# Kernel tuning notes

Measured on AMD Instinct MI355X. Metric: run time of the kernel, lower is better.

Reference implementation:

```python
import jax, jax.numpy as jnp
import numpy as np

BATCH = 65536
CHANNELS = 64
SPLIT1 = 32
SPLIT2 = 32
DEGREE = 10


def _de_casteljau(t, coeffs):
    """Evaluate Bernstein polynomials at t via De Casteljau.
    t: [N], coeffs: [N, d+1] -> [N]."""
    t = t[:, None]
    y = coeffs
    for _ in range(coeffs.shape[1] - 1):
        y = (1.0 - t) * y[:, :-1] + t * y[:, 1:]
    return y[:, 0]


def setup_inputs() -> dict:
    key = jax.random.key(0)
    k1, k2, k3 = jax.random.split(key, 3)
    x = jax.random.normal(k1, (BATCH, CHANNELS), dtype=jnp.float32)
    # subnet: Linear(SPLIT1 -> SPLIT2*(DEGREE+2)) ; W stored as [out, in] like torch
    out_dim = SPLIT2 * (DEGREE + 2)
    W = jax.random.normal(k2, (out_dim, SPLIT1), dtype=jnp.float32) * 0.05
    b = jax.random.normal(k3, (out_dim,), dtype=jnp.float32) * 0.05
    return {"x": x, "W": W, "b": b}


def reference(x, W, b):
    x1 = x[:, :SPLIT1]
    x2 = x[:, SPLIT1:]

    # subnet + reshape to per-spline params: [B*SPLIT2, DEGREE+2]
    s = (x1 @ W.T + b).reshape(-1, DEGREE + 2)
    coeff_raw = s[:, :DEGREE]
    widths = s[:, DEGREE]
    heights = s[:, DEGREE + 1]

    # monotone normalized Bernstein coefficients in [0, 1]
    cs = jnp.cumsum(jax.nn.softplus(coeff_raw), axis=-1)
    coeffs = jnp.concatenate([jnp.zeros_like(cs[:, :1]), cs], axis=-1)
    coeffs = coeffs / coeffs[:, -1:]

    widths = jax.nn.softplus(widths)
    widths = widths + 0.1 * jnp.sign(widths)
    heights = heights + 0.1 * jnp.sign(heights)

    xf = x2.reshape(-1)                    # [B*SPLIT2]
    t = xf / widths + 0.5
    tc = jnp.clip(t, 0.0, 1.0)             # l-region -> 0, r-region -> 1

    # derivative coefficients: degree * (c[1:] - c[:-1])
    deriv = DEGREE * _de_casteljau(tc, coeffs[:, 1:] - coeffs[:, :-1])
    ym = _de_casteljau(tc, coeffs)

    # branchless l / m / r regions (same math as the masked torch version)
    y = jnp.where(t < 0.0, t * deriv,
                  jnp.where(t > 1.0, 1.0 + (t - 1.0) * deriv, ym))
    y = (y - 0.5) * heights

    return jnp.concatenate([x1, y.reshape(-1, SPLIT2)], axis=1)
```

## Files before the change

kernel.cpp:

```cpp
#include <hip/hip_runtime.h>


typedef short v8s  __attribute__((ext_vector_type(8)));
typedef float f32x4 __attribute__((ext_vector_type(4)));
typedef float f32x2 __attribute__((ext_vector_type(2)));

#define LOG2E 1.44269504088896340736f
#define LN2   0.69314718055994530942f

__device__ __forceinline__ short f2bf(float f) {
    union { float f; unsigned u; } v; v.f = f;
    return (short)((v.u + 0x7FFFu + ((v.u >> 16) & 1u)) >> 16);
}

__device__ __forceinline__ float bf2f(short h) {
    union { unsigned u; float f; } v; v.u = ((unsigned)(unsigned short)h) << 16;
    return v.f;
}

__device__ __forceinline__ float sgn01(float x) {
    return (x > 0.f) ? 1.f : ((x < 0.f) ? -1.f : 0.f);
}

__device__ __forceinline__ float softplus_l2(float x) {
    return __log2f(1.0f + exp2f(x * LOG2E));
}

__device__ __forceinline__ float softplus_f(float x) {
    return __logf(1.0f + __expf(x));
}
__device__ __forceinline__ float spline_eval(const float* sv, float xf) {
    float cn[11];
    cn[0] = 0.f;
    float run = 0.f;
#pragma unroll
    for (int j = 0; j < 10; ++j) { run += softplus_f(sv[j]); cn[j + 1] = run; }
    const float inv = __fdividef(1.f, run);
    const float wd = softplus_f(sv[10]) + 0.1f;
    float hg = sv[11];
    hg += 0.1f * sgn01(hg);
    const float t   = __fdividef(xf, wd) + 0.5f;
    const float tc  = fminf(fmaxf(t, 0.f), 1.f);
#pragma unroll
    for (int n = 10; n >= 2; --n) {
#pragma unroll
        for (int i = 0; i < n; ++i) cn[i] += tc * (cn[i + 1] - cn[i]);
    }
    const float db    = cn[1] - cn[0];
    const float deriv = 10.f * db * inv;
    const float ym    = fmaf(tc, db, cn[0]) * inv;
    float y = (t < 0.f) ? (t * deriv)
            : ((t > 1.f) ? fmaf(t - 1.f, deriv, 1.f) : ym);
    return (y - 0.5f) * hg;
}

__global__ void prep_w(const float* __restrict__ W, short* __restrict__ wsH,
                       short* __restrict__ wsL) {
    const int g = blockIdx.x * 256 + threadIdx.x;
    if (g < 12288) {
        const int o = g >> 5;
        const int k = g & 31;
        const float w = W[g];
        const short hi = f2bf(w);
        const int off = (k >> 3) * 3072 + o * 8 + (k & 7);
        wsH[off] = hi;
        wsL[off] = f2bf(w - bf2f(hi));
    }
}

__global__ __launch_bounds__(256) void bern_spline_fast(
    const float* __restrict__ x, const short* __restrict__ wsH,
    const short* __restrict__ wsL, const float* __restrict__ bias,
    float* __restrict__ out)
{
    __shared__ float sl[4 * 16 * 100];

    const int tid  = threadIdx.x;
    const int wave = tid >> 6;
    const int lane = tid & 63;
    const int cbit = blockIdx.x & 1;
    const int block_row = (blockIdx.x >> 1) * 64;

    const int row16 = lane & 15;
    const int kq    = lane >> 4;
    const int arow  = block_row + wave * 16 + row16;

    const f32x4 a0 = *(const f32x4*)(x + (size_t)arow * 64 + kq * 8);
    const f32x4 a1 = *(const f32x4*)(x + (size_t)arow * 64 + kq * 8 + 4);
    v8s ah, al;
#pragma unroll
    for (int e = 0; e < 4; ++e) {
        const short h0 = f2bf(a0[e]);
        ah[e] = h0;     al[e] = f2bf(a0[e] - bf2f(h0));
        const short h1 = f2bf(a1[e]);
        ah[e + 4] = h1; al[e + 4] = f2bf(a1[e] - bf2f(h1));
    }

    float* swv = sl + wave * 1600;
    const f32x4 zero4 = {0.f, 0.f, 0.f, 0.f};

    v8s bh0[6], bl0[6];
#pragma unroll
    for (int ot = 0; ot < 6; ++ot) {
        const int boff = kq * 3072 + ((cbit * 12 + ot) * 16 + row16) * 8;
        bh0[ot] = *(const v8s*)(wsH + boff);
        bl0[ot] = *(const v8s*)(wsL + boff);
    }

#pragma unroll
    for (int ot = 0; ot < 6; ++ot) {
        f32x4 c = __builtin_amdgcn_mfma_f32_16x16x32_bf16(al, bh0[ot], zero4, 0, 0, 0);
        c = __builtin_amdgcn_mfma_f32_16x16x32_bf16(ah, bl0[ot], c, 0, 0, 0);
        c = __builtin_amdgcn_mfma_f32_16x16x32_bf16(ah, bh0[ot], c, 0, 0, 0);
#pragma unroll
        for (int r = 0; r < 4; ++r)
            swv[(kq * 4 + r) * 100 + ot * 16 + row16] = c[r];
    }

    v8s bh1[6], bl1[6];
#pragma unroll
    for (int ot = 0; ot < 6; ++ot) {
        const int boff = kq * 3072 + ((cbit * 12 + 6 + ot) * 16 + row16) * 8;
        bh1[ot] = *(const v8s*)(wsH + boff);
        bl1[ot] = *(const v8s*)(wsL + boff);
    }

#pragma unroll
    for (int hf = 0; hf < 2; ++hf) {
        if (hf == 1) {
#pragma unroll
            for (int ot = 0; ot < 6; ++ot) {
                f32x4 c = __builtin_amdgcn_mfma_f32_16x16x32_bf16(al, bh1[ot], zero4, 0, 0, 0);
                c = __builtin_amdgcn_mfma_f32_16x16x32_bf16(ah, bl1[ot], c, 0, 0, 0);
                c = __builtin_amdgcn_mfma_f32_16x16x32_bf16(ah, bh1[ot], c, 0, 0, 0);
#pragma unroll
                for (int r = 0; r < 4; ++r)
                    swv[(kq * 4 + r) * 100 + ot * 16 + row16] = c[r];
            }
        }

        const int cg0 = cbit * 16 + hf * 8 + 2 * kq;
        const f32x2 xf2 = *(const f32x2*)(x + (size_t)arow * 64 + 32 + cg0);

        const float* sp = swv + row16 * 100 + 2 * kq * 12;
        const f32x4 sA0 = *(const f32x4*)(sp);
        const f32x4 sA1 = *(const f32x4*)(sp + 4);
        const f32x4 sA2 = *(const f32x4*)(sp + 8);
        const f32x4 sB0 = *(const f32x4*)(sp + 12);
        const f32x4 sB1 = *(const f32x4*)(sp + 16);
        const f32x4 sB2 = *(const f32x4*)(sp + 20);
        const float* bp = bias + cg0 * 12;
        const f32x4 bA0 = *(const f32x4*)(bp);
        const f32x4 bA1 = *(const f32x4*)(bp + 4);
        const f32x4 bA2 = *(const f32x4*)(bp + 8);
        const f32x4 bB0 = *(const f32x4*)(bp + 12);
        const f32x4 bB1 = *(const f32x4*)(bp + 16);
        const f32x4 bB2 = *(const f32x4*)(bp + 20);

        float svA[12], svB[12];
#pragma unroll
        for (int e = 0; e < 4; ++e) {
            svA[e]     = sA0[e] + bA0[e];
            svA[e + 4] = sA1[e] + bA1[e];
            svA[e + 8] = sA2[e] + bA2[e];
            svB[e]     = sB0[e] + bB0[e];
            svB[e + 4] = sB1[e] + bB1[e];
            svB[e + 8] = sB2[e] + bB2[e];
        }

        float cnA[11], cnB[11];
        cnA[0] = 0.f; cnB[0] = 0.f;
        float runA = 0.f, runB = 0.f;
#pragma unroll
        for (int j = 0; j < 10; ++j) {
            runA += softplus_l2(svA[j]); cnA[j + 1] = runA;
            runB += softplus_l2(svB[j]); cnB[j + 1] = runB;
        }
        const float invA = __fdividef(1.f, runA);
        const float invB = __fdividef(1.f, runB);

        const float wdA = fmaf(LN2, softplus_l2(svA[10]), 0.1f);
        const float wdB = fmaf(LN2, softplus_l2(svB[10]), 0.1f);
        float hgA = svA[11]; hgA += 0.1f * sgn01(hgA);
        float hgB = svB[11]; hgB += 0.1f * sgn01(hgB);

        const float tA  = __fdividef(xf2[0], wdA) + 0.5f;
        const float tB  = __fdividef(xf2[1], wdB) + 0.5f;
        const float tcA = fminf(fmaxf(tA, 0.f), 1.f);
        const float tcB = fminf(fmaxf(tB, 0.f), 1.f);

#pragma unroll
        for (int n = 10; n >= 2; --n) {
#pragma unroll
            for (int i = 0; i < n; ++i) {
                cnA[i] += tcA * (cnA[i + 1] - cnA[i]);
                cnB[i] += tcB * (cnB[i + 1] - cnB[i]);
            }
        }
        const float dbA = cnA[1] - cnA[0];
        const float dbB = cnB[1] - cnB[0];
        const float derA = 10.f * dbA * invA;
        const float derB = 10.f * dbB * invB;
        const float ymA = fmaf(tcA, dbA, cnA[0]) * invA;
        const float ymB = fmaf(tcB, dbB, cnB[0]) * invB;

        float yA = (tA < 0.f) ? (tA * derA)
                 : ((tA > 1.f) ? fmaf(tA - 1.f, derA, 1.f) : ymA);
        float yB = (tB < 0.f) ? (tB * derB)
                 : ((tB > 1.f) ? fmaf(tB - 1.f, derB, 1.f) : ymB);

        f32x2 y2;
        y2[0] = (yA - 0.5f) * hgA;
        y2[1] = (yB - 0.5f) * hgB;
        *(f32x2*)(out + (size_t)arow * 64 + 32 + cg0) = y2;
    }

    if (cbit == 0) {
        for (int i = tid; i < 512; i += 256) {
            const int r = i >> 3, q = i & 7;
            *(f32x4*)(out + (size_t)(block_row + r) * 64 + q * 4) =
                *(const f32x4*)(x + (size_t)(block_row + r) * 64 + q * 4);
        }
    }
}

__global__ __launch_bounds__(256) void bern_spline_fallback(
    const float* __restrict__ x, const float* __restrict__ W,
    const float* __restrict__ bias, float* __restrict__ out)
{
    __shared__ short Wh[12288];
    __shared__ short Wl[12288];
    __shared__ float bl[384];
    __shared__ float sl[4 * 16 * 100];

    const int tid  = threadIdx.x;
    const int wave = tid >> 6;
    const int lane = tid & 63;
    const int block_row = blockIdx.x * 64;

    for (int g = tid; g < 12288; g += 256) {
        const int o = g >> 5;
        const int k = g & 31;
        const float w = W[g];
        const short hi = f2bf(w);
        Wh[(k >> 3) * 3072 + o * 8 + (k & 7)] = hi;
        Wl[(k >> 3) * 3072 + o * 8 + (k & 7)] = f2bf(w - bf2f(hi));
    }
    for (int g = tid; g < 384; g += 256) bl[g] = bias[g];
    __syncthreads();

    for (int i = tid; i < 512; i += 256) {
        const int r = i >> 3, q = i & 7;
        *(f32x4*)(out + (size_t)(block_row + r) * 64 + q * 4) =
            *(const f32x4*)(x + (size_t)(block_row + r) * 64 + q * 4);
    }

    const int row16 = lane & 15;
    const int kq    = lane >> 4;
    const int arow  = block_row + wave * 16 + row16;
    const f32x4 a0 = *(const f32x4*)(x + (size_t)arow * 64 + kq * 8);
    const f32x4 a1 = *(const f32x4*)(x + (size_t)arow * 64 + kq * 8 + 4);
    v8s ah, al;
#pragma unroll
    for (int e = 0; e < 4; ++e) {
        const short h0 = f2bf(a0[e]);
        ah[e] = h0;     al[e] = f2bf(a0[e] - bf2f(h0));
        const short h1 = f2bf(a1[e]);
        ah[e + 4] = h1; al[e + 4] = f2bf(a1[e] - bf2f(h1));
    }

    float* swv = sl + wave * 1600;
    const f32x4 zero4 = {0.f, 0.f, 0.f, 0.f};

    for (int qt = 0; qt < 4; ++qt) {
        f32x4 acc[6];
#pragma unroll
        for (int ot = 0; ot < 6; ++ot) {
            const int otg = qt * 6 + ot;
            const int boff = kq * 3072 + (otg * 16 + row16) * 8;
            const v8s bh  = *(const v8s*)(Wh + boff);
            const v8s blo = *(const v8s*)(Wl + boff);
            f32x4 c = __builtin_amdgcn_mfma_f32_16x16x32_bf16(al, bh, zero4, 0, 0, 0);
            c = __builtin_amdgcn_mfma_f32_16x16x32_bf16(ah, blo, c, 0, 0, 0);
            acc[ot] = __builtin_amdgcn_mfma_f32_16x16x32_bf16(ah, bh, c, 0, 0, 0);
        }
#pragma unroll
        for (int ot = 0; ot < 6; ++ot)
#pragma unroll
            for (int r = 0; r < 4; ++r)
                swv[(kq * 4 + r) * 100 + ot * 16 + row16] = acc[ot][r];

#pragma unroll
        for (int p = 0; p < 2; ++p) {
            const int idx = p * 64 + lane;
            const int cl  = idx & 7;
            const int rr  = idx >> 3;
            const int cg  = qt * 8 + cl;

            const float* sp = swv + rr * 100 + cl * 12;
            const f32x4 s0 = *(const f32x4*)(sp);
            const f32x4 s1 = *(const f32x4*)(sp + 4);
            const f32x4 s2 = *(const f32x4*)(sp + 8);
            const f32x4 b0 = *(const f32x4*)(bl + cg * 12);
            const f32x4 b1 = *(const f32x4*)(bl + cg * 12 + 4);
            const f32x4 b2 = *(const f32x4*)(bl + cg * 12 + 8);

            float sv[12];
            sv[0]  = s0[0] + b0[0]; sv[1]  = s0[1] + b0[1];
            sv[2]  = s0[2] + b0[2]; sv[3]  = s0[3] + b0[3];
            sv[4]  = s1[0] + b1[0]; sv[5]  = s1[1] + b1[1];
            sv[6]  = s1[2] + b1[2]; sv[7]  = s1[3] + b1[3];
            sv[8]  = s2[0] + b2[0]; sv[9]  = s2[1] + b2[1];
            sv[10] = s2[2] + b2[2]; sv[11] = s2[3] + b2[3];

            const int rowg = block_row + wave * 16 + rr;
            const float xf = x[(size_t)rowg * 64 + 32 + cg];
            out[(size_t)rowg * 64 + 32 + cg] = spline_eval(sv, xf);
        }
    }
}

extern "C" void kernel_launch(void* const* d_in, const int* in_sizes, int n_in,
                              void* d_out, int out_size, void* d_ws, size_t ws_size,
                              hipStream_t stream) {
    const float* x = (const float*)d_in[0];
    const float* W = (const float*)d_in[1];
    const float* b = (const float*)d_in[2];
    float* out = (float*)d_out;

    if (d_ws != nullptr && ws_size >= 49152) {
        short* wsH = (short*)d_ws;
        short* wsL = wsH + 12288;
        prep_w<<<48, 256, 0, stream>>>(W, wsH, wsL);
        bern_spline_fast<<<2048, 256, 0, stream>>>(x, wsH, wsL, b, out);
    } else {
        bern_spline_fallback<<<1024, 256, 0, stream>>>(x, W, b, out);
    }
}
```

Baseline: 34.56 us.

## Replace De Casteljau with Bernstein-Horner evaluation, fold bias into MFMA accumulator

Swaps the O(d^2) De Casteljau recursion for a Horner-style Bernstein evaluation that takes binomial weights and uses the softplus terms directly for the derivative polynomial. The bias is loaded per output column and used as the initial MFMA accumulator instead of being added after the LDS readback. The x2 loads are hoisted to the kernel start. Together these cut ALU work and global loads per spline, at the cost of some numerical-stability change from the power-basis Horner form and more live registers.

```diff
diff --git a/kernel.cpp b/kernel.cpp
--- a/kernel.cpp
+++ b/kernel.cpp
@@ -24,6 +24,44 @@
 
 __device__ __forceinline__ float softplus_l2(float x) {
     return __log2f(1.0f + exp2f(x * LOG2E));
+}
+
+__device__ __forceinline__ float spline_horner(const float* sv, float xf) {
+    float spv[10], cn_[11];
+    cn_[0] = 0.f;
+    float run = 0.f;
+#pragma unroll
+    for (int j = 0; j < 10; ++j) {
+        spv[j] = softplus_l2(sv[j]);
+        run += spv[j];
+        cn_[j + 1] = run;
+    }
+    const float inv = __fdividef(1.f, run);
+
+    const float wd = fmaf(LN2, softplus_l2(sv[10]), 0.1f);
+    float hg = sv[11];
+    hg += 0.1f * sgn01(hg);
+
+    const float t  = __fdividef(xf, wd) + 0.5f;
+    const float tc = fminf(fmaxf(t, 0.f), 1.f);
+    const float s  = 1.f - tc;
+
+    const float C10[11] = {1.f,10.f,45.f,120.f,210.f,252.f,210.f,120.f,45.f,10.f,1.f};
+    const float C9[10]  = {1.f,9.f,36.f,84.f,126.f,126.f,84.f,36.f,9.f,1.f};
+    float tk = 1.f, P = 0.f, Q = 0.f;
+#pragma unroll
+    for (int i = 0; i < 10; ++i) {
+        Q = fmaf(Q, s, tk * (C9[i] * spv[i]));
+        P = fmaf(P, s, tk * (C10[i] * cn_[i]));
+        tk *= tc;
+    }
+    P = fmaf(P, s, tk * cn_[10]);
+
+    const float der = 10.f * Q * inv;
+    const float ym  = P * inv;
+    float y = (t < 0.f) ? (t * der)
+            : ((t > 1.f) ? fmaf(t - 1.f, der, 1.f) : ym);
+    return (y - 0.5f) * hg;
 }
 
 __device__ __forceinline__ float softplus_f(float x) {
@@ -85,6 +123,10 @@
     const int kq    = lane >> 4;
     const int arow  = block_row + wave * 16 + row16;
 
+    const int cg0_h0 = cbit * 16 + 2 * kq;
+    const f32x2 xf2_0 = *(const f32x2*)(x + (size_t)arow * 64 + 32 + cg0_h0);
+    const f32x2 xf2_1 = *(const f32x2*)(x + (size_t)arow * 64 + 32 + cg0_h0 + 8);
+
     const f32x4 a0 = *(const f32x4*)(x + (size_t)arow * 64 + kq * 8);
     const f32x4 a1 = *(const f32x4*)(x + (size_t)arow * 64 + kq * 8 + 4);
     v8s ah, al;
@@ -96,8 +138,14 @@
         ah[e + 4] = h1; al[e + 4] = f2bf(a1[e] - bf2f(h1));
     }
 
+    float bv0[6], bv1[6];
+#pragma unroll
+    for (int ot = 0; ot < 6; ++ot) {
+        bv0[ot] = bias[(cbit * 12 + ot) * 16 + row16];
+        bv1[ot] = bias[(cbit * 12 + 6 + ot) * 16 + row16];
+    }
+
     float* swv = sl + wave * 1600;
-    const f32x4 zero4 = {0.f, 0.f, 0.f, 0.f};
 
     v8s bh0[6], bl0[6];
 #pragma unroll
@@ -109,7 +157,8 @@
 
 #pragma unroll
     for (int ot = 0; ot < 6; ++ot) {
-        f32x4 c = __builtin_amdgcn_mfma_f32_16x16x32_bf16(al, bh0[ot], zero4, 0, 0, 0);
+        f32x4 cb; cb[0] = bv0[ot]; cb[1] = bv0[ot]; cb[2] = bv0[ot]; cb[3] = bv0[ot];
+        f32x4 c = __builtin_amdgcn_mfma_f32_16x16x32_bf16(al, bh0[ot], cb, 0, 0, 0);
         c = __builtin_amdgcn_mfma_f32_16x16x32_bf16(ah, bl0[ot], c, 0, 0, 0);
         c = __builtin_amdgcn_mfma_f32_16x16x32_bf16(ah, bh0[ot], c, 0, 0, 0);
 #pragma unroll
@@ -130,7 +179,8 @@
         if (hf == 1) {
 #pragma unroll
             for (int ot = 0; ot < 6; ++ot) {
-                f32x4 c = __builtin_amdgcn_mfma_f32_16x16x32_bf16(al, bh1[ot], zero4, 0, 0, 0);
+                f32x4 cb; cb[0] = bv1[ot]; cb[1] = bv1[ot]; cb[2] = bv1[ot]; cb[3] = bv1[ot];
+                f32x4 c = __builtin_amdgcn_mfma_f32_16x16x32_bf16(al, bh1[ot], cb, 0, 0, 0);
                 c = __builtin_amdgcn_mfma_f32_16x16x32_bf16(ah, bl1[ot], c, 0, 0, 0);
                 c = __builtin_amdgcn_mfma_f32_16x16x32_bf16(ah, bh1[ot], c, 0, 0, 0);
 #pragma unroll
@@ -140,78 +190,29 @@
         }
 
         const int cg0 = cbit * 16 + hf * 8 + 2 * kq;
-        const f32x2 xf2 = *(const f32x2*)(x + (size_t)arow * 64 + 32 + cg0);
+        const f32x2 xf2 = (hf == 0) ? xf2_0 : xf2_1;
 
         const float* sp = swv + row16 * 100 + 2 * kq * 12;
-        const f32x4 sA0 = *(const f32x4*)(sp);
-        const f32x4 sA1 = *(const f32x4*)(sp + 4);
-        const f32x4 sA2 = *(const f32x4*)(sp + 8);
-        const f32x4 sB0 = *(const f32x4*)(sp + 12);
-        const f32x4 sB1 = *(const f32x4*)(sp + 16);
-        const f32x4 sB2 = *(const f32x4*)(sp + 20);
-        const float* bp = bias + cg0 * 12;
-        const f32x4 bA0 = *(const f32x4*)(bp);
-        const f32x4 bA1 = *(const f32x4*)(bp + 4);
-        const f32x4 bA2 = *(const f32x4*)(bp + 8);
-        const f32x4 bB0 = *(const f32x4*)(bp + 12);
-        const f32x4 bB1 = *(const f32x4*)(bp + 16);
-        const f32x4 bB2 = *(const f32x4*)(bp + 20);
-
         float svA[12], svB[12];
 #pragma unroll
         for (int e = 0; e < 4; ++e) {
-            svA[e]     = sA0[e] + bA0[e];
-            svA[e + 4] = sA1[e] + bA1[e];
-            svA[e + 8] = sA2[e] + bA2[e];
-            svB[e]     = sB0[e] + bB0[e];
-            svB[e + 4] = sB1[e] + bB1[e];
-            svB[e + 8] = sB2[e] + bB2[e];
-        }
-
-        float cnA[11], cnB[11];
-        cnA[0] = 0.f; cnB[0] = 0.f;
-        float runA = 0.f, runB = 0.f;
-#pragma unroll
-        for (int j = 0; j < 10; ++j) {
-            runA += softplus_l2(svA[j]); cnA[j + 1] = runA;
-            runB += softplus_l2(svB[j]); cnB[j + 1] = runB;
-        }
-        const float invA = __fdividef(1.f, runA);
-        const float invB = __fdividef(1.f, runB);
-
-        const float wdA = fmaf(LN2, softplus_l2(svA[10]), 0.1f);
-        const float wdB = fmaf(LN2, softplus_l2(svB[10]), 0.1f);
-        float hgA = svA[11]; hgA += 0.1f * sgn01(hgA);
-        float hgB = svB[11]; hgB += 0.1f * sgn01(hgB);
-
-        const float tA  = __fdividef(xf2[0], wdA) + 0.5f;
-        const float tB  = __fdividef(xf2[1], wdB) + 0.5f;
-        const float tcA = fminf(fmaxf(tA, 0.f), 1.f);
-        const float tcB = fminf(fmaxf(tB, 0.f), 1.f);
-
-#pragma unroll
-        for (int n = 10; n >= 2; --n) {
-#pragma unroll
-            for (int i = 0; i < n; ++i) {
-                cnA[i] += tcA * (cnA[i + 1] - cnA[i]);
-                cnB[i] += tcB * (cnB[i + 1] - cnB[i]);
-            }
-        }
-        const float dbA = cnA[1] - cnA[0];
-        const float dbB = cnB[1] - cnB[0];
-        const float derA = 10.f * dbA * invA;
-        const float derB = 10.f * dbB * invB;
-        const float ymA = fmaf(tcA, dbA, cnA[0]) * invA;
-        const float ymB = fmaf(tcB, dbB, cnB[0]) * invB;
-
-        float yA = (tA < 0.f) ? (tA * derA)
-                 : ((tA > 1.f) ? fmaf(tA - 1.f, derA, 1.f) : ymA);
-        float yB = (tB < 0.f) ? (tB * derB)
-                 : ((tB > 1.f) ? fmaf(tB - 1.f, derB, 1.f) : ymB);
+            const f32x4 vA0 = *(const f32x4*)(sp);
+            const f32x4 vA1 = *(const f32x4*)(sp + 4);
+            const f32x4 vA2 = *(const f32x4*)(sp + 8);
+            const f32x4 vB0 = *(const f32x4*)(sp + 12);
+            const f32x4 vB1 = *(const f32x4*)(sp + 16);
+            const f32x4 vB2 = *(const f32x4*)(sp + 20);
+            svA[e]     = vA0[e];
+            svA[e + 4] = vA1[e];
+            svA[e + 8] = vA2[e];
+            svB[e]     = vB0[e];
+            svB[e + 4] = vB1[e];
+            svB[e + 8] = vB2[e];
+        }
 
         f32x2 y2;
-        y2[0] = (yA - 0.5f) * hgA;
-        y2[1] = (yB - 0.5f) * hgB;
+        y2[0] = spline_horner(svA, xf2[0]);
+        y2[1] = spline_horner(svB, xf2[1]);
         *(f32x2*)(out + (size_t)arow * 64 + 32 + cg0) = y2;
     }
 
```

Result: faster. 32.21 us (-6.8%).
